# Kernel tuning notes

Measured on AMD Instinct MI355X. Metric: run time of the kernel, lower is better.

Reference implementation:

```python
import jax, jax.numpy as jnp
import numpy as np

B, H, E, G, SEQ_LEN = 131072, 64, 16, 32, 30


def setup_inputs() -> dict:
    key = jax.random.key(0)
    ks = jax.random.split(key, 17)
    def lin(kw, kb, out_f, in_f):
        s = 1.0 / np.sqrt(in_f)
        W = jax.random.uniform(kw, (out_f, in_f), jnp.float32, -s, s)
        b = jax.random.uniform(kb, (out_f,), jnp.float32, -s, s)
        return W, b
    W_se, b_se = lin(ks[0], ks[1], E, 2)
    W_h2p, b_h2p = lin(ks[2], ks[3], 2, 3 * H)
    W_goal, b_goal = lin(ks[4], ks[5], H, 2 * G)
    W_abs, b_abs = lin(ks[6], ks[7], H, 2)
    W_ih, b_ih = lin(ks[8], ks[9], 4 * H, E)
    W_hh, b_hh = lin(ks[10], ks[11], 4 * H, H)
    return {
        "traj_abs": jax.random.normal(ks[12], (1, B, 2), jnp.float32),
        "traj_rel": jax.random.normal(ks[13], (1, B, 2), jnp.float32),
        "h0": jax.random.normal(ks[14], (1, B, H), jnp.float32),
        "c0": jax.random.normal(ks[15], (1, B, H), jnp.float32),
        "goals": jax.random.normal(ks[16], (B, G, 2), jnp.float32),
        "W_ih": W_ih, "W_hh": W_hh, "b_ih": b_ih, "b_hh": b_hh,
        "W_se": W_se, "b_se": b_se,
        "W_h2p": W_h2p, "b_h2p": b_h2p,
        "W_goal": W_goal, "b_goal": b_goal,
        "W_abs": W_abs, "b_abs": b_abs,
    }


def reference(traj_abs, traj_rel, h0, c0, goals,
              W_ih, W_hh, b_ih, b_hh,
              W_se, b_se, W_h2p, b_h2p,
              W_goal, b_goal, W_abs, b_abs):
    b = traj_abs.shape[1]
    goal_emb = goals.reshape(b, -1) @ W_goal.T + b_goal            # (b, H)
    dec_in = jax.nn.leaky_relu(traj_rel[0] @ W_se.T + b_se)        # (b, E)

    def step(carry, _):
        h, c, x, abs_pos = carry
        gates = x @ W_ih.T + b_ih + h @ W_hh.T + b_hh              # (b, 4H)
        i, f, g, o = jnp.split(gates, 4, axis=-1)                  # PyTorch gate order
        c = jax.nn.sigmoid(f) * c + jax.nn.sigmoid(i) * jnp.tanh(g)
        h = jax.nn.sigmoid(o) * jnp.tanh(c)
        abs_emb = abs_pos @ W_abs.T + b_abs                        # (b, H)
        inp = jnp.concatenate([h, abs_emb, goal_emb], axis=1)      # (b, 3H)
        rel = inp @ W_h2p.T + b_h2p                                # (b, 2)
        x = jax.nn.leaky_relu(rel @ W_se.T + b_se)
        return (h, c, x, abs_pos + rel), rel

    _, rels = jax.lax.scan(step, (h0[0], c0[0], dec_in, traj_abs[0]),
                           None, length=SEQ_LEN)
    return rels  # (seq_len, b, 2)
```

## Files before the change

kernel.cpp:

```cpp
#include <hip/hip_runtime.h>
#include <stdint.h>


#define B_TOT 131072
#define SEQL 30
#define NT 4

typedef _Float16 f16x8 __attribute__((ext_vector_type(8)));
typedef _Float16 f16x2 __attribute__((ext_vector_type(2)));
typedef float f32x4 __attribute__((ext_vector_type(4)));
typedef float f32x2 __attribute__((ext_vector_type(2)));

__device__ __forceinline__ float fexp2(float x) {
#if __has_builtin(__builtin_amdgcn_exp2f)
  return __builtin_amdgcn_exp2f(x);
#else
  return exp2f(x);
#endif
}
__device__ __forceinline__ float frcp(float x) {
#if __has_builtin(__builtin_amdgcn_rcpf)
  return __builtin_amdgcn_rcpf(x);
#else
  return 1.0f / x;
#endif
}

__global__ void setup_consts(const float* __restrict__ Wgoal,
                             const float* __restrict__ bgoal,
                             const float* __restrict__ Wh2p,
                             const float* __restrict__ bh2p,
                             const float* __restrict__ Wabs,
                             const float* __restrict__ babs,
                             float* __restrict__ wsf) {
  const int tid = threadIdx.x;
  const int wv = tid >> 6;
  const int lane = tid & 63;
  if (wv == 0) {
    const int k = lane;
    float s0 = 0.f, s1 = 0.f;
#pragma unroll 8
    for (int jj = 0; jj < 64; ++jj) {
      float wg = Wgoal[jj * 64 + k];
      s0 += wg * Wh2p[128 + jj];
      s1 += wg * Wh2p[320 + jj];
    }
    wsf[k] = s0;
    wsf[64 + k] = s1;
  } else {
    const int i = lane >> 3, sub = lane & 7;
    const int p = i & 1, grp = i >> 1;
    float s = 0.f;
#pragma unroll
    for (int t = 0; t < 8; ++t) {
      int j = sub * 8 + t;
      float wv_ = (grp < 3) ? Wh2p[p * 192 + 64 + j] : Wh2p[p * 192 + 128 + j];
      float av = (grp == 0)   ? Wabs[j * 2 + 0]
                 : (grp == 1) ? Wabs[j * 2 + 1]
                 : (grp == 2) ? babs[j]
                              : bgoal[j];
      s += av * wv_;
    }
    s += __shfl_xor(s, 1, 64);
    s += __shfl_xor(s, 2, 64);
    s += __shfl_xor(s, 4, 64);
    if (sub == 0) {
      if (grp == 2) s += bh2p[p];
      wsf[128 + i] = s;
    }
  }
}

__global__ __launch_bounds__(256, 2) void lstm_mfma(
    const float* __restrict__ tabs, const float* __restrict__ trel,
    const float* __restrict__ h0, const float* __restrict__ c0,
    const float* __restrict__ goals, const float* __restrict__ Wih,
    const float* __restrict__ Whh, const float* __restrict__ bih,
    const float* __restrict__ bhh, const float* __restrict__ Wse,
    const float* __restrict__ bse, const float* __restrict__ Wh2p,
    const float* __restrict__ wsf, float* __restrict__ outp) {
  const int lane = threadIdx.x & 63;
  const int w = threadIdx.x >> 6;
  const int q = lane >> 4;
  const int n = lane & 15;
  const int pm = n & 3;
  const int hs = 16 * w;
  const int bbase = blockIdx.x * (16 * NT);

  __shared__ __align__(16) _Float16 hbuf[2 * NT * 16 * 72];

  const float SI = -1.4426950408889634f;
  const float SG = 2.8853900817779268f;
  const float gsc[4] = {SI, SI, SG, SI};
  f16x8 bw[4][3];
#pragma unroll
  for (int g = 0; g < 4; ++g) {
    const int row = g * 64 + hs + n;
    const float sc = gsc[g];
#pragma unroll
    for (int kk = 0; kk < 2; ++kk)
#pragma unroll
      for (int j = 0; j < 8; ++j)
        bw[g][kk][j] = (_Float16)(sc * Whh[row * 64 + kk * 32 + q * 8 + j]);
    float bfold = 0.f, m20 = 0.f, m21 = 0.f;
#pragma unroll
    for (int k = 0; k < 16; ++k) {
      float wik = Wih[row * 16 + k];
      bfold += bse[k] * wik;
      m20 += Wse[k * 2 + 0] * wik;
      m21 += Wse[k * 2 + 1] * wik;
    }
    float bias = sc * (bih[row] + bhh[row] + 0.505f * bfold);
#pragma unroll
    for (int j = 0; j < 8; ++j) {
      float v;
      if (q < 2)
        v = sc * Wih[row * 16 + q * 8 + j];
      else if (q == 2 && j == 0)
        v = bias;
      else if (q == 2 && j == 1)
        v = sc * 0.505f * m20;
      else if (q == 2 && j == 2)
        v = sc * 0.505f * m21;
      else
        v = 0.f;
      bw[g][2][j] = (_Float16)v;
    }
  }
  f16x8 awp0, awp1;
#pragma unroll
  for (int j = 0; j < 8; ++j) {
    float v0 = (pm < 2) ? Wh2p[pm * 192 + q * 8 + j] : 0.f;
    float v1 = (pm < 2) ? Wh2p[pm * 192 + 32 + q * 8 + j] : 0.f;
    awp0[j] = (_Float16)v0;
    awp1[j] = (_Float16)v1;
  }
  const float Sx0 = wsf[128], Sx1 = wsf[129];
  const float Sy0 = wsf[130], Sy1 = wsf[131];

  f16x2 wsaP[4], wsbP[4], bscP[4];
  const uint32_t xmask = (q < 2) ? 0x7FFF7FFFu : 0xFFFFFFFFu;
#pragma unroll
  for (int jj = 0; jj < 4; ++jj) {
    f16x2 z = f16x2{(_Float16)0.f, (_Float16)0.f};
    if (q < 2) {
      int kx = q * 8 + 2 * jj;
      wsaP[jj] =
          f16x2{(_Float16)(0.495f * Wse[kx * 2 + 0]),
                (_Float16)(0.495f * Wse[kx * 2 + 2])};
      wsbP[jj] =
          f16x2{(_Float16)(0.495f * Wse[kx * 2 + 1]),
                (_Float16)(0.495f * Wse[kx * 2 + 3])};
      bscP[jj] = f16x2{(_Float16)(0.495f * bse[kx]),
                       (_Float16)(0.495f * bse[kx + 1])};
    } else if (q == 2 && jj == 0) {
      wsaP[jj] = f16x2{(_Float16)0.f, (_Float16)1.f};
      wsbP[jj] = z;
      bscP[jj] = f16x2{(_Float16)1.f, (_Float16)0.f};
    } else if (q == 2 && jj == 1) {
      wsaP[jj] = z;
      wsbP[jj] = f16x2{(_Float16)1.f, (_Float16)0.f};
      bscP[jj] = z;
    } else {
      wsaP[jj] = z;
      wsbP[jj] = z;
      bscP[jj] = z;
    }
  }

  auto build_x = [&](float r0f, float r1f) -> f16x8 {
    f16x2 r0h = f16x2{(_Float16)r0f, (_Float16)r0f};
    f16x2 r1h = f16x2{(_Float16)r1f, (_Float16)r1f};
    f16x8 xr;
#pragma unroll
    for (int jj = 0; jj < 4; ++jj) {
      f16x2 t = r0h * wsaP[jj] + (r1h * wsbP[jj] + bscP[jj]);
      uint32_t tu = __builtin_bit_cast(uint32_t, t) & xmask;
      f16x2 lr = __builtin_bit_cast(f16x2, tu);
      xr[2 * jj] = lr[0];
      xr[2 * jj + 1] = lr[1];
    }
    return xr;
  };

  const f32x4 zC = {0.f, 0.f, 0.f, 0.f};

  float Gg0[NT], Gg1[NT];
  float ax[NT], ay[NT], cst[NT][4];
  f16x8 xf[NT];
  {
    f16x8 aM0, aM1;
#pragma unroll
    for (int j = 0; j < 8; ++j) {
      int k = q * 8 + j;
      aM0[j] = (_Float16)((pm < 2) ? wsf[pm * 64 + k] : 0.f);
      aM1[j] = (_Float16)((pm < 2) ? wsf[pm * 64 + 32 + k] : 0.f);
    }
    const float Sb0 = wsf[132] + wsf[134];
    const float Sb1 = wsf[133] + wsf[135];
#pragma unroll
    for (int t = 0; t < NT; ++t) {
      const int bb = bbase + 16 * t;
      f16x8 bg0, bg1;
#pragma unroll
      for (int j = 0; j < 8; ++j) {
        int k = q * 8 + j;
        bg0[j] = (_Float16)goals[(bb + n) * 64 + k];
        bg1[j] = (_Float16)goals[(bb + n) * 64 + 32 + k];
      }
      f32x4 Ga = __builtin_amdgcn_mfma_f32_16x16x32_f16(aM0, bg0, zC, 0, 0, 0);
      Ga = __builtin_amdgcn_mfma_f32_16x16x32_f16(aM1, bg1, Ga, 0, 0, 0);
      Gg0[t] = Ga[0] + Sb0;
      Gg1[t] = Ga[1] + Sb1;

      ax[t] = tabs[(bb + n) * 2 + 0];
      ay[t] = tabs[(bb + n) * 2 + 1];
#pragma unroll
      for (int r = 0; r < 4; ++r) {
        const int b = bb + 4 * q + r;
        cst[t][r] = c0[b * 64 + hs + n];
        hbuf[t * 1152 + (4 * q + r) * 72 + hs + n] =
            (_Float16)h0[b * 64 + hs + n];
      }
      xf[t] = build_x(trel[(bb + n) * 2 + 0], trel[(bb + n) * 2 + 1]);
    }
  }

  const int ro = n * 72 + q * 8;
  const int wo = (4 * q) * 72 + hs + n;
  const float K2 = 2.8853900817779268f;

  int poff = 0;
  for (int s = 0; s <= SEQL; ++s) {
    __syncthreads();

#pragma unroll
    for (int p2 = 0; p2 < NT / 2; ++p2) {
      f16x8 ah0[2], ah1[2];
#pragma unroll
      for (int u = 0; u < 2; ++u) {
        const int t = 2 * p2 + u;
        ah0[u] = *(const f16x8*)(hbuf + poff + t * 1152 + ro);
        ah1[u] = *(const f16x8*)(hbuf + poff + t * 1152 + ro + 32);
      }

      if (s > 0) {
#pragma unroll
        for (int u = 0; u < 2; ++u) {
          const int t = 2 * p2 + u;
          f32x4 p = __builtin_amdgcn_mfma_f32_16x16x32_f16(awp0, ah0[u], zC,
                                                           0, 0, 0);
          p = __builtin_amdgcn_mfma_f32_16x16x32_f16(awp1, ah1[u], p, 0, 0, 0);
          float u0 = p[0] + Gg0[t] + fmaf(ax[t], Sx0, ay[t] * Sy0);
          float u1 = p[1] + Gg1[t] + fmaf(ax[t], Sx1, ay[t] * Sy1);
          ax[t] += u0;
          ay[t] += u1;
          if (w == t && lane < 16) {
            float2 v;
            v.x = u0;
            v.y = u1;
            ((float2*)outp)[(size_t)(s - 1) * B_TOT + bbase + 16 * t + lane] =
                v;
          }
          xf[t] = build_x(u0, u1);
        }
      }

      if (s < SEQL) {
        f32x4 acc[2][4];
#pragma unroll
        for (int g = 0; g < 4; ++g)
#pragma unroll
          for (int u = 0; u < 2; ++u) {
            const int t = 2 * p2 + u;
            f32x4 a = __builtin_amdgcn_mfma_f32_16x16x32_f16(ah0[u], bw[g][0],
                                                             zC, 0, 0, 0);
            a = __builtin_amdgcn_mfma_f32_16x16x32_f16(ah1[u], bw[g][1], a,
                                                       0, 0, 0);
            a = __builtin_amdgcn_mfma_f32_16x16x32_f16(xf[t], bw[g][2], a,
                                                       0, 0, 0);
            acc[u][g] = a;
          }
#pragma unroll
        for (int u = 0; u < 2; ++u) {
          const int t = 2 * p2 + u;
          _Float16* hw = hbuf + (poff ^ 4608) + t * 1152 + wo;
#pragma unroll
          for (int pr = 0; pr < 2; ++pr) {
            const int ra = 2 * pr, rb = 2 * pr + 1;
            f32x2 Av = {fexp2(acc[u][0][ra]), fexp2(acc[u][0][rb])};
            f32x2 Fv = {fexp2(acc[u][1][ra]), fexp2(acc[u][1][rb])};
            f32x2 Bv = {fexp2(acc[u][2][ra]), fexp2(acc[u][2][rb])};
            const f32x2 one = {1.f, 1.f};
            f32x2 t1 = Av + one;
            f32x2 t2 = Bv + one;
            f32x2 t3 = Fv + one;
            f32x2 t4 = Bv - one;
            f32x2 m1 = t1 * t2;
            f32x2 cs = {cst[t][ra], cst[t][rb]};
            f32x2 num = cs * m1 + t4 * t3;
            f32x2 den = m1 * t3;
            float Rc = frcp(den[0] * den[1]);
            float cc0 = num[0] * den[1] * Rc;
            float cc1 = num[1] * den[0] * Rc;
            cst[t][ra] = cc0;
            cst[t][rb] = cc1;
            f32x2 Cv = {fexp2(acc[u][3][ra]), fexp2(acc[u][3][rb])};
            f32x2 Dv = {fexp2(K2 * cc0), fexp2(K2 * cc1)};
            f32x2 hd = (Cv + one) * (Dv + one);
            f32x2 hnm = Dv - one;
            float Rh = frcp(hd[0] * hd[1]);
            hw[72 * ra] = (_Float16)(hnm[0] * hd[1] * Rh);
            hw[72 * rb] = (_Float16)(hnm[1] * hd[0] * Rh);
          }
        }
      }
    }
    if (s < SEQL) poff ^= 4608;
  }
}

extern "C" void kernel_launch(void* const* d_in, const int* in_sizes, int n_in,
                              void* d_out, int out_size, void* d_ws,
                              size_t ws_size, hipStream_t stream) {
  (void)in_sizes; (void)n_in; (void)out_size; (void)ws_size;
  const float* tabs  = (const float*)d_in[0];
  const float* trel  = (const float*)d_in[1];
  const float* h0    = (const float*)d_in[2];
  const float* c0    = (const float*)d_in[3];
  const float* goals = (const float*)d_in[4];
  const float* Wih   = (const float*)d_in[5];
  const float* Whh   = (const float*)d_in[6];
  const float* bih   = (const float*)d_in[7];
  const float* bhh   = (const float*)d_in[8];
  const float* Wse   = (const float*)d_in[9];
  const float* bse   = (const float*)d_in[10];
  const float* Wh2p  = (const float*)d_in[11];
  const float* bh2p  = (const float*)d_in[12];
  const float* Wgoal = (const float*)d_in[13];
  const float* bgoal = (const float*)d_in[14];
  const float* Wabs  = (const float*)d_in[15];
  const float* babs  = (const float*)d_in[16];
  float* wsf = (float*)d_ws;

  setup_consts<<<dim3(1), dim3(128), 0, stream>>>(Wgoal, bgoal, Wh2p, bh2p,
                                                  Wabs, babs, wsf);
  lstm_mfma<<<dim3(B_TOT / (16 * NT)), dim3(256), 0, stream>>>(
      tabs, trel, h0, c0, goals, Wih, Whh, bih, bhh, Wse, bse, Wh2p, wsf,
      (float*)d_out);
}
```

Baseline: 468.1 us.

## Move LSTM weights to swizzled LDS and split batch tiles across 8 waves

Recurrent and input weight fragments move from per-thread registers into XOR-swizzled shared memory and are reloaded each step. The block grows to 512 threads, with two wave groups each owning two of the four 16-row batch tiles, so per-thread state is halved. The hidden-state buffer switches from padded rows to an XOR swizzle. The goal is fewer registers per thread and more resident waves to hide MFMA and transcendental latency, at the cost of extra LDS reads every step and higher LDS use per block.

```diff
diff --git a/kernel.cpp b/kernel.cpp
--- a/kernel.cpp
+++ b/kernel.cpp
@@ -71,7 +71,7 @@
   }
 }
 
-__global__ __launch_bounds__(256, 2) void lstm_mfma(
+__global__ __launch_bounds__(512, 4) void lstm_mfma(
     const float* __restrict__ tabs, const float* __restrict__ trel,
     const float* __restrict__ h0, const float* __restrict__ c0,
     const float* __restrict__ goals, const float* __restrict__ Wih,
@@ -81,52 +81,57 @@
     const float* __restrict__ wsf, float* __restrict__ outp) {
   const int lane = threadIdx.x & 63;
   const int w = threadIdx.x >> 6;
+  const int wsl = w & 3;
+  const int tp = w >> 2;
   const int q = lane >> 4;
   const int n = lane & 15;
   const int pm = n & 3;
-  const int hs = 16 * w;
+  const int hs = 16 * wsl;
   const int bbase = blockIdx.x * (16 * NT);
 
-  __shared__ __align__(16) _Float16 hbuf[2 * NT * 16 * 72];
+  __shared__ __align__(16) _Float16 whh[4 * 64 * 64];
+  __shared__ __align__(16) _Float16 wx[4 * 64 * 32];
+  __shared__ __align__(16) _Float16 hbuf[2 * NT * 16 * 64];
 
   const float SI = -1.4426950408889634f;
   const float SG = 2.8853900817779268f;
-  const float gsc[4] = {SI, SI, SG, SI};
-  f16x8 bw[4][3];
-#pragma unroll
-  for (int g = 0; g < 4; ++g) {
-    const int row = g * 64 + hs + n;
-    const float sc = gsc[g];
-#pragma unroll
-    for (int kk = 0; kk < 2; ++kk)
-#pragma unroll
-      for (int j = 0; j < 8; ++j)
-        bw[g][kk][j] = (_Float16)(sc * Whh[row * 64 + kk * 32 + q * 8 + j]);
+
+  for (int idx = threadIdx.x; idx < 4 * 64 * 64; idx += 512) {
+    const int r = idx >> 6, k = idx & 63;
+    const float sc = ((r >> 6) == 2) ? SG : SI;
+    const int slot = (k >> 3) ^ (r & 7);
+    whh[r * 64 + slot * 8 + (k & 7)] = (_Float16)(sc * Whh[r * 64 + k]);
+  }
+  if (threadIdx.x < 256) {
+    const int r = threadIdx.x;
+    const float sc = ((r >> 6) == 2) ? SG : SI;
     float bfold = 0.f, m20 = 0.f, m21 = 0.f;
 #pragma unroll
     for (int k = 0; k < 16; ++k) {
-      float wik = Wih[row * 16 + k];
+      float wik = Wih[r * 16 + k];
       bfold += bse[k] * wik;
       m20 += Wse[k * 2 + 0] * wik;
       m21 += Wse[k * 2 + 1] * wik;
     }
-    float bias = sc * (bih[row] + bhh[row] + 0.505f * bfold);
-#pragma unroll
-    for (int j = 0; j < 8; ++j) {
+    const float bias = sc * (bih[r] + bhh[r] + 0.505f * bfold);
+#pragma unroll
+    for (int kx = 0; kx < 32; ++kx) {
       float v;
-      if (q < 2)
-        v = sc * Wih[row * 16 + q * 8 + j];
-      else if (q == 2 && j == 0)
+      if (kx < 16)
+        v = sc * Wih[r * 16 + kx];
+      else if (kx == 16)
         v = bias;
-      else if (q == 2 && j == 1)
+      else if (kx == 17)
         v = sc * 0.505f * m20;
-      else if (q == 2 && j == 2)
+      else if (kx == 18)
         v = sc * 0.505f * m21;
       else
         v = 0.f;
-      bw[g][2][j] = (_Float16)v;
-    }
-  }
+      const int slot = (kx >> 3) ^ (r & 3);
+      wx[r * 32 + slot * 8 + (kx & 7)] = (_Float16)v;
+    }
+  }
+
   f16x8 awp0, awp1;
 #pragma unroll
   for (int j = 0; j < 8; ++j) {
@@ -145,12 +150,10 @@
     f16x2 z = f16x2{(_Float16)0.f, (_Float16)0.f};
     if (q < 2) {
       int kx = q * 8 + 2 * jj;
-      wsaP[jj] =
-          f16x2{(_Float16)(0.495f * Wse[kx * 2 + 0]),
-                (_Float16)(0.495f * Wse[kx * 2 + 2])};
-      wsbP[jj] =
-          f16x2{(_Float16)(0.495f * Wse[kx * 2 + 1]),
-                (_Float16)(0.495f * Wse[kx * 2 + 3])};
+      wsaP[jj] = f16x2{(_Float16)(0.495f * Wse[kx * 2 + 0]),
+                       (_Float16)(0.495f * Wse[kx * 2 + 2])};
+      wsbP[jj] = f16x2{(_Float16)(0.495f * Wse[kx * 2 + 1]),
+                       (_Float16)(0.495f * Wse[kx * 2 + 3])};
       bscP[jj] = f16x2{(_Float16)(0.495f * bse[kx]),
                        (_Float16)(0.495f * bse[kx + 1])};
     } else if (q == 2 && jj == 0) {
@@ -185,9 +188,9 @@
 
   const f32x4 zC = {0.f, 0.f, 0.f, 0.f};
 
-  float Gg0[NT], Gg1[NT];
-  float ax[NT], ay[NT], cst[NT][4];
-  f16x8 xf[NT];
+  float Gg0[2], Gg1[2];
+  float ax[2], ay[2], cst[2][4];
+  f16x8 xf[2];
   {
     f16x8 aM0, aM1;
 #pragma unroll
@@ -199,8 +202,9 @@
     const float Sb0 = wsf[132] + wsf[134];
     const float Sb1 = wsf[133] + wsf[135];
 #pragma unroll
-    for (int t = 0; t < NT; ++t) {
-      const int bb = bbase + 16 * t;
+    for (int u = 0; u < 2; ++u) {
+      const int tg = 2 * tp + u;
+      const int bb = bbase + 16 * tg;
       f16x8 bg0, bg1;
 #pragma unroll
       for (int j = 0; j < 8; ++j) {
@@ -210,113 +214,119 @@
       }
       f32x4 Ga = __builtin_amdgcn_mfma_f32_16x16x32_f16(aM0, bg0, zC, 0, 0, 0);
       Ga = __builtin_amdgcn_mfma_f32_16x16x32_f16(aM1, bg1, Ga, 0, 0, 0);
-      Gg0[t] = Ga[0] + Sb0;
-      Gg1[t] = Ga[1] + Sb1;
-
-      ax[t] = tabs[(bb + n) * 2 + 0];
-      ay[t] = tabs[(bb + n) * 2 + 1];
+      Gg0[u] = Ga[0] + Sb0;
+      Gg1[u] = Ga[1] + Sb1;
+
+      ax[u] = tabs[(bb + n) * 2 + 0];
+      ay[u] = tabs[(bb + n) * 2 + 1];
+      const int cslot = (hs + n) >> 3, cin = n & 7;
 #pragma unroll
       for (int r = 0; r < 4; ++r) {
-        const int b = bb + 4 * q + r;
-        cst[t][r] = c0[b * 64 + hs + n];
-        hbuf[t * 1152 + (4 * q + r) * 72 + hs + n] =
+        const int row = 4 * q + r;
+        const int b = bb + row;
+        cst[u][r] = c0[b * 64 + hs + n];
+        hbuf[tg * 1024 + row * 64 + ((cslot ^ (row & 7)) << 3) + cin] =
             (_Float16)h0[b * 64 + hs + n];
       }
-      xf[t] = build_x(trel[(bb + n) * 2 + 0], trel[(bb + n) * 2 + 1]);
-    }
-  }
-
-  const int ro = n * 72 + q * 8;
-  const int wo = (4 * q) * 72 + hs + n;
+      xf[u] = build_x(trel[(bb + n) * 2 + 0], trel[(bb + n) * 2 + 1]);
+    }
+  }
+
+  const int ro0 = n * 64 + ((q ^ (n & 7)) << 3);
+  const int ro1 = n * 64 + (((4 + q) ^ (n & 7)) << 3);
+  const int hb = (hs + n) * 64;
+  const int sl0 = (q ^ (n & 7)) << 3;
+  const int sl1 = (((4 + q) ^ (n & 7))) << 3;
+  const int xb = (hs + n) * 32 + ((q ^ (n & 3)) << 3);
+  const int wslot = (hs + n) >> 3, wcin = n & 7;
+
   const float K2 = 2.8853900817779268f;
 
   int poff = 0;
   for (int s = 0; s <= SEQL; ++s) {
     __syncthreads();
-
-#pragma unroll
-    for (int p2 = 0; p2 < NT / 2; ++p2) {
-      f16x8 ah0[2], ah1[2];
+    f16x8 ah0[2], ah1[2];
+#pragma unroll
+    for (int u = 0; u < 2; ++u) {
+      const int tb = poff + (2 * tp + u) * 1024;
+      ah0[u] = *(const f16x8*)(hbuf + tb + ro0);
+      ah1[u] = *(const f16x8*)(hbuf + tb + ro1);
+    }
+
+    if (s > 0) {
 #pragma unroll
       for (int u = 0; u < 2; ++u) {
-        const int t = 2 * p2 + u;
-        ah0[u] = *(const f16x8*)(hbuf + poff + t * 1152 + ro);
-        ah1[u] = *(const f16x8*)(hbuf + poff + t * 1152 + ro + 32);
-      }
-
-      if (s > 0) {
+        f32x4 p = __builtin_amdgcn_mfma_f32_16x16x32_f16(awp0, ah0[u], zC,
+                                                         0, 0, 0);
+        p = __builtin_amdgcn_mfma_f32_16x16x32_f16(awp1, ah1[u], p, 0, 0, 0);
+        float u0 = p[0] + Gg0[u] + fmaf(ax[u], Sx0, ay[u] * Sy0);
+        float u1 = p[1] + Gg1[u] + fmaf(ax[u], Sx1, ay[u] * Sy1);
+        ax[u] += u0;
+        ay[u] += u1;
+        if (wsl == u && lane < 16) {
+          float2 v;
+          v.x = u0;
+          v.y = u1;
+          ((float2*)outp)[(size_t)(s - 1) * B_TOT + bbase + 16 * (2 * tp + u) +
+                          lane] = v;
+        }
+        xf[u] = build_x(u0, u1);
+      }
+    }
+
+    if (s < SEQL) {
+      f32x4 acc[2][4];
+#pragma unroll
+      for (int g = 0; g < 4; ++g) {
+        const f16x8 w0 = *(const f16x8*)(whh + g * 4096 + hb + sl0);
+        const f16x8 w1 = *(const f16x8*)(whh + g * 4096 + hb + sl1);
+        const f16x8 w2 = *(const f16x8*)(wx + g * 2048 + xb);
 #pragma unroll
         for (int u = 0; u < 2; ++u) {
-          const int t = 2 * p2 + u;
-          f32x4 p = __builtin_amdgcn_mfma_f32_16x16x32_f16(awp0, ah0[u], zC,
+          f32x4 a = __builtin_amdgcn_mfma_f32_16x16x32_f16(ah0[u], w0, zC,
                                                            0, 0, 0);
-          p = __builtin_amdgcn_mfma_f32_16x16x32_f16(awp1, ah1[u], p, 0, 0, 0);
-          float u0 = p[0] + Gg0[t] + fmaf(ax[t], Sx0, ay[t] * Sy0);
-          float u1 = p[1] + Gg1[t] + fmaf(ax[t], Sx1, ay[t] * Sy1);
-          ax[t] += u0;
-          ay[t] += u1;
-          if (w == t && lane < 16) {
-            float2 v;
-            v.x = u0;
-            v.y = u1;
-            ((float2*)outp)[(size_t)(s - 1) * B_TOT + bbase + 16 * t + lane] =
-                v;
-          }
-          xf[t] = build_x(u0, u1);
+          a = __builtin_amdgcn_mfma_f32_16x16x32_f16(ah1[u], w1, a, 0, 0, 0);
+          a = __builtin_amdgcn_mfma_f32_16x16x32_f16(xf[u], w2, a, 0, 0, 0);
+          acc[u][g] = a;
         }
       }
-
-      if (s < SEQL) {
-        f32x4 acc[2][4];
-#pragma unroll
-        for (int g = 0; g < 4; ++g)
-#pragma unroll
-          for (int u = 0; u < 2; ++u) {
-            const int t = 2 * p2 + u;
-            f32x4 a = __builtin_amdgcn_mfma_f32_16x16x32_f16(ah0[u], bw[g][0],
-                                                             zC, 0, 0, 0);
-            a = __builtin_amdgcn_mfma_f32_16x16x32_f16(ah1[u], bw[g][1], a,
-                                                       0, 0, 0);
-            a = __builtin_amdgcn_mfma_f32_16x16x32_f16(xf[t], bw[g][2], a,
-                                                       0, 0, 0);
-            acc[u][g] = a;
-          }
-#pragma unroll
-        for (int u = 0; u < 2; ++u) {
-          const int t = 2 * p2 + u;
-          _Float16* hw = hbuf + (poff ^ 4608) + t * 1152 + wo;
-#pragma unroll
-          for (int pr = 0; pr < 2; ++pr) {
-            const int ra = 2 * pr, rb = 2 * pr + 1;
-            f32x2 Av = {fexp2(acc[u][0][ra]), fexp2(acc[u][0][rb])};
-            f32x2 Fv = {fexp2(acc[u][1][ra]), fexp2(acc[u][1][rb])};
-            f32x2 Bv = {fexp2(acc[u][2][ra]), fexp2(acc[u][2][rb])};
-            const f32x2 one = {1.f, 1.f};
-            f32x2 t1 = Av + one;
-            f32x2 t2 = Bv + one;
-            f32x2 t3 = Fv + one;
-            f32x2 t4 = Bv - one;
-            f32x2 m1 = t1 * t2;
-            f32x2 cs = {cst[t][ra], cst[t][rb]};
-            f32x2 num = cs * m1 + t4 * t3;
-            f32x2 den = m1 * t3;
-            float Rc = frcp(den[0] * den[1]);
-            float cc0 = num[0] * den[1] * Rc;
-            float cc1 = num[1] * den[0] * Rc;
-            cst[t][ra] = cc0;
-            cst[t][rb] = cc1;
-            f32x2 Cv = {fexp2(acc[u][3][ra]), fexp2(acc[u][3][rb])};
-            f32x2 Dv = {fexp2(K2 * cc0), fexp2(K2 * cc1)};
-            f32x2 hd = (Cv + one) * (Dv + one);
-            f32x2 hnm = Dv - one;
-            float Rh = frcp(hd[0] * hd[1]);
-            hw[72 * ra] = (_Float16)(hnm[0] * hd[1] * Rh);
-            hw[72 * rb] = (_Float16)(hnm[1] * hd[0] * Rh);
-          }
+#pragma unroll
+      for (int u = 0; u < 2; ++u) {
+        _Float16* hw = hbuf + (poff ^ 4096) + (2 * tp + u) * 1024;
+#pragma unroll
+        for (int pr = 0; pr < 2; ++pr) {
+          const int ra = 2 * pr, rb = 2 * pr + 1;
+          f32x2 Av = {fexp2(acc[u][0][ra]), fexp2(acc[u][0][rb])};
+          f32x2 Fv = {fexp2(acc[u][1][ra]), fexp2(acc[u][1][rb])};
+          f32x2 Bv = {fexp2(acc[u][2][ra]), fexp2(acc[u][2][rb])};
+          const f32x2 one = {1.f, 1.f};
+          f32x2 t1 = Av + one;
+          f32x2 t2 = Bv + one;
+          f32x2 t3 = Fv + one;
+          f32x2 t4 = Bv - one;
+          f32x2 m1 = t1 * t2;
+          f32x2 cs = {cst[u][ra], cst[u][rb]};
+          f32x2 num = cs * m1 + t4 * t3;
+          f32x2 den = m1 * t3;
+          float Rc = frcp(den[0] * den[1]);
+          float cc0 = num[0] * den[1] * Rc;
+          float cc1 = num[1] * den[0] * Rc;
+          cst[u][ra] = cc0;
+          cst[u][rb] = cc1;
+          f32x2 Cv = {fexp2(acc[u][3][ra]), fexp2(acc[u][3][rb])};
+          f32x2 Dv = {fexp2(K2 * cc0), fexp2(K2 * cc1)};
+          f32x2 hd = (Cv + one) * (Dv + one);
+          f32x2 hnm = Dv - one;
+          float Rh = frcp(hd[0] * hd[1]);
+          float h0v = hnm[0] * hd[1] * Rh;
+          float h1v = hnm[1] * hd[0] * Rh;
+          const int rowa = 4 * q + ra, rowb = 4 * q + rb;
+          hw[rowa * 64 + ((wslot ^ (rowa & 7)) << 3) + wcin] = (_Float16)h0v;
+          hw[rowb * 64 + ((wslot ^ (rowb & 7)) << 3) + wcin] = (_Float16)h1v;
         }
       }
-    }
-    if (s < SEQL) poff ^= 4608;
+      poff ^= 4096;
+    }
   }
 }
 
@@ -345,7 +355,7 @@
 
   setup_consts<<<dim3(1), dim3(128), 0, stream>>>(Wgoal, bgoal, Wh2p, bh2p,
                                                   Wabs, babs, wsf);
-  lstm_mfma<<<dim3(B_TOT / (16 * NT)), dim3(256), 0, stream>>>(
+  lstm_mfma<<<dim3(B_TOT / (16 * NT)), dim3(512), 0, stream>>>(
       tabs, trel, h0, c0, goals, Wih, Whh, bih, bhh, Wse, bse, Wh2p, wsf,
       (float*)d_out);
 }
```

Measured after the change: 468.9 us. No clear change (+0.2%).
